# Performance work log

Measured on AMD Instinct MI355X. Metric: run time of the kernel, lower is better.

The kernel has to match this reference:

```python
import jax, jax.numpy as jnp
import numpy as np

N = 40000          # nodes
E = 400000         # edges (avg degree 10)
MUL0, MUL1 = 64, 32   # 64x0e + 32x1o
RAD, HID = 8, 64      # fc_neurons = [8, 64]
WNUM = 192            # tp.weight_numel = 64+64+32+32
NUM_NEIGHBORS = 10.0
INV3 = 1.0 / np.sqrt(3.0)   # wigner coeff for 1o x 1o -> 0e


def _lin(s, v, Ws, Wv, attr):
    """FullyConnectedTensorProduct(x, 1x0e attr) == per-irrep linear, fan-in normalized."""
    out_s = (s @ Ws) * attr * (1.0 / np.sqrt(Ws.shape[0]))
    out_v = jnp.einsum('nud,uv->nvd', v, Wv) * attr[..., None] * (1.0 / np.sqrt(Wv.shape[0]))
    return out_s, out_v


def setup_inputs() -> dict:
    key = jax.random.key(0)
    ks = jax.random.split(key, 16)
    return {
        'node_input':   jax.random.normal(ks[0], (N, MUL0 + 3 * MUL1), jnp.float32),
        'node_attr':    jnp.ones((N, 1), jnp.float32),
        'edge_attr':    jax.random.normal(ks[1], (E, 4), jnp.float32),   # 1x0e + 1x1o
        'edge_scalars': jax.random.uniform(ks[2], (E, RAD), jnp.float32),
        'W_sc_s': jax.random.normal(ks[3], (MUL0, MUL0), jnp.float32),
        'W_sc_v': jax.random.normal(ks[4], (MUL1, MUL1), jnp.float32),
        'W1_s':   jax.random.normal(ks[5], (MUL0, MUL0), jnp.float32),
        'W1_v':   jax.random.normal(ks[6], (MUL1, MUL1), jnp.float32),
        'W2_s':   jax.random.normal(ks[7], (MUL0 + MUL1, MUL0), jnp.float32),
        'W2_v':   jax.random.normal(ks[8], (MUL0 + MUL1, MUL1), jnp.float32),
        'W3':     jax.random.normal(ks[9], (MUL0 + MUL1, 1), jnp.float32),
        'fcW1':   jax.random.normal(ks[10], (RAD, HID), jnp.float32),
        'fcW2':   jax.random.normal(ks[11], (HID, WNUM), jnp.float32),
        'edge_src': jax.random.randint(ks[12], (E,), 0, N, jnp.int32),
        'edge_dst': jax.random.randint(ks[13], (E,), 0, N, jnp.int32),
    }


def reference(node_input, node_attr, edge_attr, edge_scalars,
              W_sc_s, W_sc_v, W1_s, W1_v, W2_s, W2_v, W3, fcW1, fcW2,
              edge_src, edge_dst):
    n = node_input.shape[0]
    s_in = node_input[:, :MUL0]                       # (N, 64)   0e
    v_in = node_input[:, MUL0:].reshape(n, MUL1, 3)   # (N, 32,3) 1o

    # self connection + first linear (FCTP with 1x0e attr)
    sc_s, sc_v = _lin(s_in, v_in, W_sc_s, W_sc_v, node_attr)
    f_s,  f_v  = _lin(s_in, v_in, W1_s,  W1_v,  node_attr)

    # radial MLP -> per-edge tensor-product weights (silu, fan-in normalized)
    h = jax.nn.silu(edge_scalars @ fcW1 * (1.0 / np.sqrt(RAD)))
    w = h @ fcW2 * (1.0 / np.sqrt(HID))               # (E, 192)
    wA, wB, wC, wD = w[:, :64], w[:, 64:128], w[:, 128:160], w[:, 160:192]

    # gather source node features
    xs = f_s[edge_src]                                # (E, 64)
    xv = f_v[edge_src]                                # (E, 32, 3)
    y0 = edge_attr[:, :1]                             # (E, 1)  0e
    y1 = edge_attr[:, 1:4]                            # (E, 3)  1o

    # 'uvu' tensor-product paths -> irreps_mid = 64x0e + 32x0e + 64x1o + 32x1o
    outA = wA * xs * y0                                            # 0e x 0e -> 0e
    outD = wD * jnp.einsum('eud,ed->eu', xv, y1) * INV3            # 1o x 1o -> 0e
    outB = wB[:, :, None] * xs[:, :, None] * y1[:, None, :]       # 0e x 1o -> 1o
    outC = wC[:, :, None] * xv * y0[:, :, None]                    # 1o x 0e -> 1o
    edge_feat = jnp.concatenate(
        [outA, outD, outB.reshape(-1, MUL0 * 3), outC.reshape(-1, MUL1 * 3)], axis=1)  # (E, 384)

    # scatter_add into destination nodes, normalized by sqrt(num_neighbors)
    agg = jax.ops.segment_sum(edge_feat, edge_dst, num_segments=n)
    agg = agg * (1.0 / np.sqrt(NUM_NEIGHBORS))

    ms = agg[:, :MUL0 + MUL1]                               # (N, 96)   0e
    mv = agg[:, MUL0 + MUL1:].reshape(n, MUL0 + MUL1, 3)    # (N, 96,3) 1o

    # lin2: mid -> output ; lin3: mid -> 0e (scalars only)
    c_s, c_v = _lin(ms, mv, W2_s, W2_v, node_attr)
    conv = jnp.concatenate([c_s, c_v.reshape(n, -1)], axis=1)
    sc   = jnp.concatenate([sc_s, sc_v.reshape(n, -1)], axis=1)
    angle = 0.1 * (ms @ W3) * node_attr * (1.0 / np.sqrt(MUL0 + MUL1))  # (N, 1)

    # sc.output_mask is all-ones here (every output irrep has a path)
    cos, sin = jnp.cos(angle), jnp.sin(angle)
    return cos * sc + sin * conv
```

## Files before the change

### kernel.cpp

```cpp
#include <hip/hip_runtime.h>
#include <math.h>

#define MUL0 64
#define MUL1 32
#define RADF 8
#define HIDF 64
#define WNUM 192
#define NODE_F 160
#define AGG_F  384

#define INV_SQRT64 0.125f
#define INV_SQRT32 0.17677669529663687f
#define INV_SQRT8  0.35355339059327373f
#define INV_SQRT96 0.10206207261596575f
#define INV_SQRT10 0.31622776601683794f
#define INV_SQRT3  0.5773502691896258f

typedef __attribute__((ext_vector_type(8))) short bf16x8;
typedef __attribute__((ext_vector_type(4))) float f32x4;

__device__ __forceinline__ float bf2f(unsigned short u) {
    return __uint_as_float((unsigned)u << 16);
}
__device__ __forceinline__ unsigned short f2bfu(float x) {
    unsigned ua = __float_as_uint(x);
    return (unsigned short)((ua + 0x7FFF + ((ua >> 16) & 1)) >> 16);
}
__device__ __forceinline__ unsigned bf16pack(float a, float b) {
    unsigned ua = __float_as_uint(a);
    unsigned ub = __float_as_uint(b);
    ua = (ua + 0x7FFF + ((ua >> 16) & 1)) >> 16;
    ub = (ub + 0x7FFF + ((ub >> 16) & 1)) >> 16;
    return ua | (ub << 16);
}
__device__ __forceinline__ int rdlane(int v, int i) {
    return __builtin_amdgcn_readlane(v, i);
}
__device__ __forceinline__ float rdlanef(float v, int i) {
    return __int_as_float(__builtin_amdgcn_readlane(__float_as_int(v), i));
}
__device__ __forceinline__ bf16x8 cvt8(float4 a, float4 b) {
    union { unsigned q[4]; bf16x8 v; } r;
    r.q[0] = bf16pack(a.x, a.y);
    r.q[1] = bf16pack(a.z, a.w);
    r.q[2] = bf16pack(b.x, b.y);
    r.q[3] = bf16pack(b.z, b.w);
    return r.v;
}

__global__ __launch_bounds__(256) void k_node_lin(
    const float* __restrict__ node_input,
    const float* __restrict__ node_attr,
    const float* __restrict__ W1_s,
    const float* __restrict__ W1_v,
    unsigned short* __restrict__ f, int N)
{
    __shared__ unsigned short s_w1s[8 * 64 * 8];
    __shared__ unsigned short s_w1v[4 * 32 * 8];
    int tid = threadIdx.x;

    for (int task = tid; task < 8 * 64; task += 256) {
        int col = task & 63, koct = task >> 6;
        const float* wp = W1_s + (size_t)(koct * 8) * MUL0 + col;
        unsigned pk0 = bf16pack(wp[0 * MUL0] * INV_SQRT64, wp[1 * MUL0] * INV_SQRT64);
        unsigned pk1 = bf16pack(wp[2 * MUL0] * INV_SQRT64, wp[3 * MUL0] * INV_SQRT64);
        unsigned pk2 = bf16pack(wp[4 * MUL0] * INV_SQRT64, wp[5 * MUL0] * INV_SQRT64);
        unsigned pk3 = bf16pack(wp[6 * MUL0] * INV_SQRT64, wp[7 * MUL0] * INV_SQRT64);
        *(uint4*)&s_w1s[task * 8] = make_uint4(pk0, pk1, pk2, pk3);
    }
    for (int task = tid; task < 4 * 32; task += 256) {
        int col = task & 31, koct = task >> 5;
        const float* wp = W1_v + (size_t)(koct * 8) * MUL1 + col;
        unsigned pk0 = bf16pack(wp[0 * MUL1] * INV_SQRT32, wp[1 * MUL1] * INV_SQRT32);
        unsigned pk1 = bf16pack(wp[2 * MUL1] * INV_SQRT32, wp[3 * MUL1] * INV_SQRT32);
        unsigned pk2 = bf16pack(wp[4 * MUL1] * INV_SQRT32, wp[5 * MUL1] * INV_SQRT32);
        unsigned pk3 = bf16pack(wp[6 * MUL1] * INV_SQRT32, wp[7 * MUL1] * INV_SQRT32);
        *(uint4*)&s_w1v[task * 8] = make_uint4(pk0, pk1, pk2, pk3);
    }
    __syncthreads();

    int lane = tid & 63;
    int wv = tid >> 6;
    int l15 = lane & 15, lh = lane >> 4;
    int ntiles = (N + 15) >> 4;

    for (int tile = blockIdx.x * 4 + wv; tile < ntiles; tile += gridDim.x * 4) {
        int n0 = tile << 4;
        int m = min(16, N - n0);
        int nrow = n0 + min(l15, m - 1);
        const float* inn = node_input + (size_t)nrow * NODE_F;

        float attr[4];
        #pragma unroll
        for (int r = 0; r < 4; ++r)
            attr[r] = node_attr[n0 + min(lh * 4 + r, m - 1)];

        bf16x8 inS[2];
        #pragma unroll
        for (int kk = 0; kk < 2; ++kk) {
            const float* p0 = inn + kk * 32 + lh * 8;
            inS[kk] = cvt8(*(const float4*)p0, *(const float4*)(p0 + 4));
        }
        #pragma unroll
        for (int cb = 0; cb < 4; ++cb) {
            f32x4 a = {0.f, 0.f, 0.f, 0.f};
            #pragma unroll
            for (int kk = 0; kk < 2; ++kk) {
                bf16x8 b = *(const bf16x8*)&s_w1s[(((kk * 4 + lh) * 64) + cb * 16 + l15) * 8];
                a = __builtin_amdgcn_mfma_f32_16x16x32_bf16(inS[kk], b, a, 0, 0, 0);
            }
            #pragma unroll
            for (int r = 0; r < 4; ++r) {
                int node = lh * 4 + r;
                if (node < m)
                    f[(size_t)(n0 + node) * NODE_F + cb * 16 + l15] = f2bfu(a[r] * attr[r]);
            }
        }

        #pragma unroll
        for (int d = 0; d < 3; ++d) {
            float t[8];
            #pragma unroll
            for (int j = 0; j < 8; ++j)
                t[j] = inn[64 + (lh * 8 + j) * 3 + d];
            bf16x8 inV = cvt8(make_float4(t[0], t[1], t[2], t[3]),
                              make_float4(t[4], t[5], t[6], t[7]));
            #pragma unroll
            for (int cb = 0; cb < 2; ++cb) {
                bf16x8 b = *(const bf16x8*)&s_w1v[((lh * 32) + cb * 16 + l15) * 8];
                f32x4 a = {0.f, 0.f, 0.f, 0.f};
                a = __builtin_amdgcn_mfma_f32_16x16x32_bf16(inV, b, a, 0, 0, 0);
                #pragma unroll
                for (int r = 0; r < 4; ++r) {
                    int node = lh * 4 + r;
                    if (node < m)
                        f[(size_t)(n0 + node) * NODE_F + 64 + d * 32 + cb * 16 + l15] =
                            f2bfu(a[r] * attr[r]);
                }
            }
        }
    }
}

__global__ void k_count(const int* __restrict__ edge_dst, int* deg, int E)
{
    int e = blockIdx.x * blockDim.x + threadIdx.x;
    if (e < E) atomicAdd(&deg[edge_dst[e]], 1);
}

__global__ __launch_bounds__(1024) void k_scan(const int* __restrict__ deg,
                                               int* __restrict__ off,
                                               int* __restrict__ cur, int N)
{
    __shared__ int swsum[16];
    __shared__ int swoff[16];
    __shared__ int sbase;
    __shared__ int stotal;
    int lane = threadIdx.x & 63, wid = threadIdx.x >> 6;
    if (threadIdx.x == 0) sbase = 0;
    __syncthreads();
    int ngroups = N >> 2;
    for (int base = 0; base < ngroups; base += 1024) {
        int g = base + threadIdx.x;
        int4 v = make_int4(0, 0, 0, 0);
        if (g < ngroups) v = ((const int4*)deg)[g];
        int s = v.x + v.y + v.z + v.w;
        int val = s;
        #pragma unroll
        for (int sh = 1; sh < 64; sh <<= 1) {
            int t = __shfl_up(val, sh);
            if (lane >= sh) val += t;
        }
        if (lane == 63) swsum[wid] = val;
        __syncthreads();
        if (threadIdx.x < 16) {
            int x = swsum[threadIdx.x];
            int xv = x;
            #pragma unroll
            for (int sh = 1; sh < 16; sh <<= 1) {
                int t = __shfl_up(xv, sh);
                if ((int)threadIdx.x >= sh) xv += t;
            }
            swoff[threadIdx.x] = xv - x;
            if (threadIdx.x == 15) stotal = xv;
        }
        __syncthreads();
        if (g < ngroups) {
            int b = sbase + swoff[wid] + (val - s);
            int4 o;
            o.x = b; o.y = b + v.x; o.z = o.y + v.y; o.w = o.z + v.z;
            ((int4*)off)[g] = o;
            ((int4*)cur)[g] = o;
        }
        __syncthreads();
        if (threadIdx.x == 0) sbase += stotal;
        __syncthreads();
    }
    if (threadIdx.x == 0) {
        int b = sbase;
        for (int i = (ngroups << 2); i < N; ++i) { off[i] = b; cur[i] = b; b += deg[i]; }
        off[N] = b;
    }
}

__global__ void k_scatter(const int* __restrict__ edge_dst,
                          int* cur, int* __restrict__ csr, int E)
{
    int e = blockIdx.x * blockDim.x + threadIdx.x;
    if (e < E) {
        int d = edge_dst[e];
        int pos = atomicAdd(&cur[d], 1);
        csr[pos] = e;
    }
}

#define FLUSH_AGG(node, AT)                                          \
    do {                                                             \
        float* an = agg + (size_t)(node) * AGG_F;                    \
        if (AT) {                                                    \
            atomicAdd(&an[lane], accA);                              \
            atomicAdd(&an[96  + lane], accB0);                       \
            atomicAdd(&an[192 + lane], accB1);                       \
            atomicAdd(&an[288 + lane], accB2);                       \
            if (lane < 32) {                                         \
                atomicAdd(&an[160 + u], accX0);                      \
                atomicAdd(&an[256 + u], accX1);                      \
                atomicAdd(&an[352 + u], accX2);                      \
            } else {                                                 \
                atomicAdd(&an[64 + u], accX0);                       \
            }                                                        \
        } else {                                                     \
            an[lane] = accA;                                         \
            an[96  + lane] = accB0;                                  \
            an[192 + lane] = accB1;                                  \
            an[288 + lane] = accB2;                                  \
            if (lane < 32) {                                         \
                an[160 + u] = accX0;                                 \
                an[256 + u] = accX1;                                 \
                an[352 + u] = accX2;                                 \
            } else {                                                 \
                an[64 + u] = accX0;                                  \
            }                                                        \
        }                                                            \
    } while (0)

__global__ __launch_bounds__(256, 3) void k_edge_fused(
    const unsigned short* __restrict__ f,
    const float* __restrict__ edge_scalars,
    const float* __restrict__ edge_attr,
    const float* __restrict__ fcW1,
    const float* __restrict__ fcW2,
    const int* __restrict__ edge_src,
    const int* __restrict__ edge_dst,
    const int* __restrict__ csr,
    const int* __restrict__ off,
    float* agg, int E)
{
    __shared__ unsigned short s_w2t[8 * 192 * 8];
    __shared__ unsigned short s_w[4][16 * 216];
    __shared__ float s_fcW1[512];

    int tid  = threadIdx.x;
    int lane = tid & 63;
    int wv   = tid >> 6;
    int l15  = lane & 15, lh = lane >> 4;
    int u    = lane & 31;

    for (int task = tid; task < 1536; task += 256) {
        int col = task % 192, oct = task / 192;
        const float* wp = fcW2 + (size_t)(oct * 8) * WNUM + col;
        unsigned pk0 = bf16pack(wp[0 * WNUM], wp[1 * WNUM]);
        unsigned pk1 = bf16pack(wp[2 * WNUM], wp[3 * WNUM]);
        unsigned pk2 = bf16pack(wp[4 * WNUM], wp[5 * WNUM]);
        unsigned pk3 = bf16pack(wp[6 * WNUM], wp[7 * WNUM]);
        *(uint4*)&s_w2t[oct * 1536 + col * 8] = make_uint4(pk0, pk1, pk2, pk3);
    }
    for (int i = tid; i < 512; i += 256)
        s_fcW1[i] = fcW1[i];
    __syncthreads();

    unsigned short* sw = s_w[wv];
    int nwt = (E + 15) >> 4;
    int stride4 = gridDim.x * 4;

    int wt = blockIdx.x * 4 + wv;
    if (wt >= nwt) return;

    int P = wt << 4;
    int m = min(16, E - P);
    int e0 = csr[P + min(l15, m - 1)];
    int src = edge_src[e0];
    int dst = edge_dst[e0];
    float4 ea = *(const float4*)(edge_attr + (size_t)e0 * 4);
    float4 es0, es1;
    {
        const float4* esp = (const float4*)(edge_scalars + (size_t)e0 * RADF);
        es0 = esp[0]; es1 = esp[1];
    }

    while (true) {
        int firstd = rdlane(dst, 0);
        int lastd  = rdlane(dst, m - 1);
        int off_first = off[firstd];
        int off_last  = off[lastd + 1];

        int wt_n = wt + stride4;
        bool hn = wt_n < nwt;
        int P_n = hn ? (wt_n << 4) : 0;
        int m_n = hn ? min(16, E - P_n) : 1;

        int e_n = csr[hn ? (P_n + min(l15, m_n - 1)) : 0];

        float xs[16], xv0[16], xv1[16], xv2[16];
        #pragma unroll
        for (int i = 0; i < 16; ++i) {
            int si = rdlane(src, i);
            const unsigned short* fb = f + (size_t)si * NODE_F;
            xs[i]  = bf2f(fb[lane]);
            xv0[i] = bf2f(fb[64 + u]);
            xv1[i] = bf2f(fb[96 + u]);
            xv2[i] = bf2f(fb[128 + u]);
        }

        float es[8] = {es0.x, es0.y, es0.z, es0.w, es1.x, es1.y, es1.z, es1.w};
        union { unsigned q[4]; bf16x8 v; } A0, A1;
        #pragma unroll
        for (int jp = 0; jp < 4; ++jp) {
            int k0 = lh * 8 + 2 * jp;
            float aL0 = 0.f, aL1 = 0.f, aH0 = 0.f, aH1 = 0.f;
            #pragma unroll
            for (int r = 0; r < 8; ++r) {
                float2 wl = *(const float2*)&s_fcW1[r * 64 + k0];
                float2 wh = *(const float2*)&s_fcW1[r * 64 + 32 + k0];
                aL0 = fmaf(es[r], wl.x, aL0);
                aL1 = fmaf(es[r], wl.y, aL1);
                aH0 = fmaf(es[r], wh.x, aH0);
                aH1 = fmaf(es[r], wh.y, aH1);
            }
            aL0 *= INV_SQRT8; aL1 *= INV_SQRT8; aH0 *= INV_SQRT8; aH1 *= INV_SQRT8;
            aL0 = aL0 / (1.f + __expf(-aL0));
            aL1 = aL1 / (1.f + __expf(-aL1));
            aH0 = aH0 / (1.f + __expf(-aH0));
            aH1 = aH1 / (1.f + __expf(-aH1));
            A0.q[jp] = bf16pack(aL0, aL1);
            A1.q[jp] = bf16pack(aH0, aH1);
        }

        int src_n = edge_src[e_n];
        int dst_n = edge_dst[e_n];
        float4 ea_n = *(const float4*)(edge_attr + (size_t)e_n * 4);
        float4 es0_n, es1_n;
        {
            const float4* espn = (const float4*)(edge_scalars + (size_t)e_n * RADF);
            es0_n = espn[0]; es1_n = espn[1];
        }

        #pragma unroll
        for (int cb = 0; cb < 12; ++cb) {
            bf16x8 b0 = *(const bf16x8*)&s_w2t[ lh      * 1536 + (cb * 16 + l15) * 8];
            bf16x8 b1 = *(const bf16x8*)&s_w2t[(4 + lh) * 1536 + (cb * 16 + l15) * 8];
            f32x4 acc = {0.f, 0.f, 0.f, 0.f};
            acc = __builtin_amdgcn_mfma_f32_16x16x32_bf16(A0.v, b0, acc, 0, 0, 0);
            acc = __builtin_amdgcn_mfma_f32_16x16x32_bf16(A1.v, b1, acc, 0, 0, 0);
            #pragma unroll
            for (int r = 0; r < 4; ++r)
                sw[(lh * 4 + r) * 216 + cb * 16 + l15] = f2bfu(acc[r] * INV_SQRT64);
        }

        float accA = 0.f, accB0 = 0.f, accB1 = 0.f, accB2 = 0.f;
        float accX0 = 0.f, accX1 = 0.f, accX2 = 0.f;
        int curd = rdlane(dst, 0);
        #pragma unroll
        for (int i = 0; i < 16; ++i) {
            if (i < m) {
                int di = rdlane(dst, i);
                if (di != curd) {
                    bool at = (curd == firstd) && (off_first < P);
                    FLUSH_AGG(curd, at);
                    accA = accB0 = accB1 = accB2 = 0.f;
                    accX0 = accX1 = accX2 = 0.f;
                    curd = di;
                }
                float eax = rdlanef(ea.x, i);
                float eay = rdlanef(ea.y, i);
                float eaz = rdlanef(ea.z, i);
                float eaw = rdlanef(ea.w, i);
                float W0 = bf2f(sw[i * 216 + lane]);
                float W1 = bf2f(sw[i * 216 + 64 + lane]);
                float W2 = bf2f(sw[i * 216 + 128 + lane]);
                accA = fmaf(W0 * xs[i], eax, accA);
                float bx = W1 * xs[i];
                accB0 = fmaf(bx, eay, accB0);
                accB1 = fmaf(bx, eaz, accB1);
                accB2 = fmaf(bx, eaw, accB2);
                if (lane < 32) {
                    float cc = W2 * eax;
                    accX0 = fmaf(cc, xv0[i], accX0);
                    accX1 = fmaf(cc, xv1[i], accX1);
                    accX2 = fmaf(cc, xv2[i], accX2);
                } else {
                    float dv = xv0[i] * eay + xv1[i] * eaz + xv2[i] * eaw;
                    accX0 = fmaf(W2 * INV_SQRT3, dv, accX0);
                }
            }
        }
        {
            bool at_fin = ((curd == firstd) && (off_first < P)) || (off_last > P + m);
            FLUSH_AGG(curd, at_fin);
        }

        if (!hn) break;
        wt = wt_n; P = P_n; m = m_n;
        src = src_n; dst = dst_n; ea = ea_n; es0 = es0_n; es1 = es1_n;
    }
}

__global__ __launch_bounds__(256) void k_out(
    const float* __restrict__ node_input,
    const float* __restrict__ node_attr,
    const float* __restrict__ agg,
    const float* __restrict__ W_sc_s,
    const float* __restrict__ W_sc_v,
    const float* __restrict__ W2_s,
    const float* __restrict__ W2_v,
    const float* __restrict__ W3,
    float* __restrict__ out, int N)
{
    __shared__ unsigned short s_w2s[12 * 64 * 8];
    __shared__ unsigned short s_wss[ 8 * 64 * 8];
    __shared__ unsigned short s_w2v[12 * 32 * 8];
    __shared__ unsigned short s_wsv[ 4 * 32 * 8];
    __shared__ unsigned short s_w3 [12 * 16 * 8];

    const float pre = INV_SQRT10 * INV_SQRT96;
    int tid = threadIdx.x;

    for (int task = tid; task < 12 * 64; task += 256) {
        int col = task & 63, koct = task >> 6;
        const float* wp = W2_s + (size_t)(koct * 8) * MUL0 + col;
        unsigned pk0 = bf16pack(wp[0 * MUL0] * pre, wp[1 * MUL0] * pre);
        unsigned pk1 = bf16pack(wp[2 * MUL0] * pre, wp[3 * MUL0] * pre);
        unsigned pk2 = bf16pack(wp[4 * MUL0] * pre, wp[5 * MUL0] * pre);
        unsigned pk3 = bf16pack(wp[6 * MUL0] * pre, wp[7 * MUL0] * pre);
        *(uint4*)&s_w2s[task * 8] = make_uint4(pk0, pk1, pk2, pk3);
    }
    for (int task = tid; task < 8 * 64; task += 256) {
        int col = task & 63, koct = task >> 6;
        const float* wp = W_sc_s + (size_t)(koct * 8) * MUL0 + col;
        unsigned pk0 = bf16pack(wp[0 * MUL0] * INV_SQRT64, wp[1 * MUL0] * INV_SQRT64);
        unsigned pk1 = bf16pack(wp[2 * MUL0] * INV_SQRT64, wp[3 * MUL0] * INV_SQRT64);
        unsigned pk2 = bf16pack(wp[4 * MUL0] * INV_SQRT64, wp[5 * MUL0] * INV_SQRT64);
        unsigned pk3 = bf16pack(wp[6 * MUL0] * INV_SQRT64, wp[7 * MUL0] * INV_SQRT64);
        *(uint4*)&s_wss[task * 8] = make_uint4(pk0, pk1, pk2, pk3);
    }
    for (int task = tid; task < 12 * 32; task += 256) {
        int col = task & 31, koct = task >> 5;
        const float* wp = W2_v + (size_t)(koct * 8) * MUL1 + col;
        unsigned pk0 = bf16pack(wp[0 * MUL1] * pre, wp[1 * MUL1] * pre);
        unsigned pk1 = bf16pack(wp[2 * MUL1] * pre, wp[3 * MUL1] * pre);
        unsigned pk2 = bf16pack(wp[4 * MUL1] * pre, wp[5 * MUL1] * pre);
        unsigned pk3 = bf16pack(wp[6 * MUL1] * pre, wp[7 * MUL1] * pre);
        *(uint4*)&s_w2v[task * 8] = make_uint4(pk0, pk1, pk2, pk3);
    }
    for (int task = tid; task < 4 * 32; task += 256) {
        int col = task & 31, koct = task >> 5;
        const float* wp = W_sc_v + (size_t)(koct * 8) * MUL1 + col;
        unsigned pk0 = bf16pack(wp[0 * MUL1] * INV_SQRT32, wp[1 * MUL1] * INV_SQRT32);
        unsigned pk1 = bf16pack(wp[2 * MUL1] * INV_SQRT32, wp[3 * MUL1] * INV_SQRT32);
        unsigned pk2 = bf16pack(wp[4 * MUL1] * INV_SQRT32, wp[5 * MUL1] * INV_SQRT32);
        unsigned pk3 = bf16pack(wp[6 * MUL1] * INV_SQRT32, wp[7 * MUL1] * INV_SQRT32);
        *(uint4*)&s_wsv[task * 8] = make_uint4(pk0, pk1, pk2, pk3);
    }
    for (int task = tid; task < 12 * 16; task += 256) {
        int col = task & 15, koct = task >> 4;
        const float sc3 = 0.1f * pre;
        unsigned pk0 = 0, pk1 = 0, pk2 = 0, pk3 = 0;
        if (col == 0) {
            const float* wp = W3 + koct * 8;
            pk0 = bf16pack(wp[0] * sc3, wp[1] * sc3);
            pk1 = bf16pack(wp[2] * sc3, wp[3] * sc3);
            pk2 = bf16pack(wp[4] * sc3, wp[5] * sc3);
            pk3 = bf16pack(wp[6] * sc3, wp[7] * sc3);
        }
        *(uint4*)&s_w3[task * 8] = make_uint4(pk0, pk1, pk2, pk3);
    }
    __syncthreads();

    int lane = tid & 63;
    int wv = tid >> 6;
    int l15 = lane & 15, lh = lane >> 4;
    int ntiles = (N + 15) >> 4;

    for (int tile = blockIdx.x * 4 + wv; tile < ntiles; tile += gridDim.x * 4) {
        int n0 = tile << 4;
        int m = min(16, N - n0);
        int nrow = n0 + min(l15, m - 1);
        const float* agn = agg + (size_t)nrow * AGG_F;
        const float* inn = node_input + (size_t)nrow * NODE_F;

        bf16x8 aggA[3], inS[2];
        #pragma unroll
        for (int kk = 0; kk < 3; ++kk) {
            const float* p0 = agn + kk * 32 + lh * 8;
            aggA[kk] = cvt8(*(const float4*)p0, *(const float4*)(p0 + 4));
        }
        #pragma unroll
        for (int kk = 0; kk < 2; ++kk) {
            const float* p0 = inn + kk * 32 + lh * 8;
            inS[kk] = cvt8(*(const float4*)p0, *(const float4*)(p0 + 4));
        }

        f32x4 convS[4], scS[4], angD = {0.f, 0.f, 0.f, 0.f};
        #pragma unroll
        for (int cb = 0; cb < 4; ++cb) {
            f32x4 a = {0.f, 0.f, 0.f, 0.f};
            #pragma unroll
            for (int kk = 0; kk < 3; ++kk) {
                bf16x8 b = *(const bf16x8*)&s_w2s[(((kk * 4 + lh) * 64) + cb * 16 + l15) * 8];
                a = __builtin_amdgcn_mfma_f32_16x16x32_bf16(aggA[kk], b, a, 0, 0, 0);
            }
            convS[cb] = a;
            f32x4 s = {0.f, 0.f, 0.f, 0.f};
            #pragma unroll
            for (int kk = 0; kk < 2; ++kk) {
                bf16x8 b = *(const bf16x8*)&s_wss[(((kk * 4 + lh) * 64) + cb * 16 + l15) * 8];
                s = __builtin_amdgcn_mfma_f32_16x16x32_bf16(inS[kk], b, s, 0, 0, 0);
            }
            scS[cb] = s;
        }
        #pragma unroll
        for (int kk = 0; kk < 3; ++kk) {
            bf16x8 b = *(const bf16x8*)&s_w3[(((kk * 4 + lh) * 16) + l15) * 8];
            angD = __builtin_amdgcn_mfma_f32_16x16x32_bf16(aggA[kk], b, angD, 0, 0, 0);
        }

        float attr[4], cs[4], sn[4];
        #pragma unroll
        for (int r = 0; r < 4; ++r) {
            attr[r] = node_attr[n0 + min(lh * 4 + r, m - 1)];
            float ang = __shfl(angD[r], lane & 48) * attr[r];
            cs[r] = cosf(ang);
            sn[r] = sinf(ang);
        }

        #pragma unroll
        for (int cb = 0; cb < 4; ++cb)
            #pragma unroll
            for (int r = 0; r < 4; ++r) {
                int node = lh * 4 + r;
                if (node < m)
                    out[(size_t)(n0 + node) * NODE_F + cb * 16 + l15] =
                        attr[r] * (cs[r] * scS[cb][r] + sn[r] * convS[cb][r]);
            }

        #pragma unroll
        for (int d = 0; d < 3; ++d) {
            bf16x8 aggV[3], inV;
            #pragma unroll
            for (int kk = 0; kk < 3; ++kk) {
                const float* p0 = agn + 96 + d * 96 + kk * 32 + lh * 8;
                aggV[kk] = cvt8(*(const float4*)p0, *(const float4*)(p0 + 4));
            }
            {
                float t[8];
                #pragma unroll
                for (int j = 0; j < 8; ++j)
                    t[j] = inn[64 + (lh * 8 + j) * 3 + d];
                inV = cvt8(make_float4(t[0], t[1], t[2], t[3]),
                           make_float4(t[4], t[5], t[6], t[7]));
            }
            #pragma unroll
            for (int cb = 0; cb < 2; ++cb) {
                f32x4 a = {0.f, 0.f, 0.f, 0.f};
                #pragma unroll
                for (int kk = 0; kk < 3; ++kk) {
                    bf16x8 b = *(const bf16x8*)&s_w2v[(((kk * 4 + lh) * 32) + cb * 16 + l15) * 8];
                    a = __builtin_amdgcn_mfma_f32_16x16x32_bf16(aggV[kk], b, a, 0, 0, 0);
                }
                f32x4 s = {0.f, 0.f, 0.f, 0.f};
                {
                    bf16x8 b = *(const bf16x8*)&s_wsv[((lh * 32) + cb * 16 + l15) * 8];
                    s = __builtin_amdgcn_mfma_f32_16x16x32_bf16(inV, b, s, 0, 0, 0);
                }
                #pragma unroll
                for (int r = 0; r < 4; ++r) {
                    int node = lh * 4 + r;
                    if (node < m)
                        out[(size_t)(n0 + node) * NODE_F + 64 + (cb * 16 + l15) * 3 + d] =
                            attr[r] * (cs[r] * s[r] + sn[r] * a[r]);
                }
            }
        }
    }
}

extern "C" void kernel_launch(void* const* d_in, const int* in_sizes, int n_in,
                              void* d_out, int out_size, void* d_ws, size_t ws_size,
                              hipStream_t stream)
{
    const float* node_input   = (const float*)d_in[0];
    const float* node_attr    = (const float*)d_in[1];
    const float* edge_attr    = (const float*)d_in[2];
    const float* edge_scalars = (const float*)d_in[3];
    const float* W_sc_s       = (const float*)d_in[4];
    const float* W_sc_v       = (const float*)d_in[5];
    const float* W1_s         = (const float*)d_in[6];
    const float* W1_v         = (const float*)d_in[7];
    const float* W2_s         = (const float*)d_in[8];
    const float* W2_v         = (const float*)d_in[9];
    const float* W3           = (const float*)d_in[10];
    const float* fcW1         = (const float*)d_in[11];
    const float* fcW2         = (const float*)d_in[12];
    const int*   edge_src     = (const int*)d_in[13];
    const int*   edge_dst     = (const int*)d_in[14];
    float* out = (float*)d_out;

    const int N = in_sizes[1];
    const int E = in_sizes[13];

    char* p = (char*)d_ws;
    float* agg = (float*)p;            p += (size_t)N * AGG_F * sizeof(float);
    unsigned short* fbf = (unsigned short*)p;  p += (size_t)N * NODE_F * sizeof(unsigned short);
    int*   deg = (int*)p;              p += (size_t)N * sizeof(int);
    int*   cur = (int*)p;              p += (size_t)N * sizeof(int);
    int*   csr = (int*)p;              p += (size_t)E * sizeof(int);
    int*   off = (int*)p;              p += (size_t)(N + 1) * sizeof(int);

    hipMemsetAsync(deg, 0, (size_t)N * sizeof(int), stream);
    hipMemsetAsync(agg, 0, (size_t)N * AGG_F * sizeof(float), stream);

    int eb = (E + 255) / 256;
    k_count<<<eb, 256, 0, stream>>>(edge_dst, deg, E);
    k_scan<<<1, 1024, 0, stream>>>(deg, off, cur, N);
    k_scatter<<<eb, 256, 0, stream>>>(edge_dst, cur, csr, E);

    int ntiles = (N + 15) / 16;
    int gridL = (ntiles + 3) / 4;
    k_node_lin<<<gridL, 256, 0, stream>>>(node_input, node_attr, W1_s, W1_v, fbf, N);

    int nwt = (E + 15) / 16;
    int gridF = (nwt + 3) / 4;
    if (gridF > 1536) gridF = 1536;
    k_edge_fused<<<gridF, 256, 0, stream>>>(fbf, edge_scalars, edge_attr, fcW1, fcW2,
                                            edge_src, edge_dst, csr, off, agg, E);

    int gridO = (ntiles + 3) / 4;
    if (gridO > 640) gridO = 640;
    k_out<<<gridO, 256, 0, stream>>>(node_input, node_attr, agg,
                                     W_sc_s, W_sc_v, W2_s, W2_v, W3, out, N);
}
```

Before: 239.1 us.

## Align edge work tiles to destination boundaries to drop atomics and agg memset

```diff
diff --git a/kernel.cpp b/kernel.cpp
--- a/kernel.cpp
+++ b/kernel.cpp
@@ -148,58 +148,82 @@
     if (e < E) atomicAdd(&deg[edge_dst[e]], 1);
 }
 
-__global__ __launch_bounds__(1024) void k_scan(const int* __restrict__ deg,
-                                               int* __restrict__ off,
-                                               int* __restrict__ cur, int N)
+__global__ __launch_bounds__(1024) void k_scan_a(const int* __restrict__ deg,
+                                                 int* __restrict__ off,
+                                                 int* __restrict__ bsum, int N)
 {
     __shared__ int swsum[16];
     __shared__ int swoff[16];
+    __shared__ int stot;
+    int lane = threadIdx.x & 63, wid = threadIdx.x >> 6;
+    int ng4 = (N + 3) >> 2;
+    int g = blockIdx.x * 1024 + threadIdx.x;
+    int4 v = make_int4(0, 0, 0, 0);
+    if (g < ng4) v = ((const int4*)deg)[g];
+    int s = v.x + v.y + v.z + v.w;
+    int val = s;
+    #pragma unroll
+    for (int sh = 1; sh < 64; sh <<= 1) {
+        int t = __shfl_up(val, sh);
+        if (lane >= sh) val += t;
+    }
+    if (lane == 63) swsum[wid] = val;
+    __syncthreads();
+    if (threadIdx.x < 16) {
+        int x = swsum[threadIdx.x];
+        int xv = x;
+        #pragma unroll
+        for (int sh = 1; sh < 16; sh <<= 1) {
+            int t = __shfl_up(xv, sh);
+            if ((int)threadIdx.x >= sh) xv += t;
+        }
+        swoff[threadIdx.x] = xv - x;
+        if (threadIdx.x == 15) stot = xv;
+    }
+    __syncthreads();
+    if (g < ng4) {
+        int b0 = swoff[wid] + (val - s);
+        int4 o;
+        o.x = b0; o.y = b0 + v.x; o.z = o.y + v.y; o.w = o.z + v.z;
+        ((int4*)off)[g] = o;
+    }
+    if (threadIdx.x == 0) bsum[blockIdx.x] = stot;
+}
+
+__global__ __launch_bounds__(1024) void k_scan_b(int* __restrict__ off,
+                                                 int* __restrict__ cur,
+                                                 const int* __restrict__ bsum,
+                                                 float* __restrict__ agg,
+                                                 const int* __restrict__ deg,
+                                                 int N, int nb)
+{
     __shared__ int sbase;
-    __shared__ int stotal;
-    int lane = threadIdx.x & 63, wid = threadIdx.x >> 6;
-    if (threadIdx.x == 0) sbase = 0;
+    if (threadIdx.x == 0) {
+        int s = 0;
+        for (int j = 0; j < (int)blockIdx.x; ++j) s += bsum[j];
+        sbase = s;
+    }
     __syncthreads();
-    int ngroups = N >> 2;
-    for (int base = 0; base < ngroups; base += 1024) {
-        int g = base + threadIdx.x;
-        int4 v = make_int4(0, 0, 0, 0);
-        if (g < ngroups) v = ((const int4*)deg)[g];
-        int s = v.x + v.y + v.z + v.w;
-        int val = s;
-        #pragma unroll
-        for (int sh = 1; sh < 64; sh <<= 1) {
-            int t = __shfl_up(val, sh);
-            if (lane >= sh) val += t;
-        }
-        if (lane == 63) swsum[wid] = val;
-        __syncthreads();
-        if (threadIdx.x < 16) {
-            int x = swsum[threadIdx.x];
-            int xv = x;
-            #pragma unroll
-            for (int sh = 1; sh < 16; sh <<= 1) {
-                int t = __shfl_up(xv, sh);
-                if ((int)threadIdx.x >= sh) xv += t;
-            }
-            swoff[threadIdx.x] = xv - x;
-            if (threadIdx.x == 15) stotal = xv;
-        }
-        __syncthreads();
-        if (g < ngroups) {
-            int b = sbase + swoff[wid] + (val - s);
-            int4 o;
-            o.x = b; o.y = b + v.x; o.z = o.y + v.y; o.w = o.z + v.z;
-            ((int4*)off)[g] = o;
-            ((int4*)cur)[g] = o;
-        }
-        __syncthreads();
-        if (threadIdx.x == 0) sbase += stotal;
-        __syncthreads();
-    }
-    if (threadIdx.x == 0) {
-        int b = sbase;
-        for (int i = (ngroups << 2); i < N; ++i) { off[i] = b; cur[i] = b; b += deg[i]; }
-        off[N] = b;
+    int base = sbase;
+    int ng4 = (N + 3) >> 2;
+    int g = blockIdx.x * 1024 + threadIdx.x;
+    if (g < ng4) {
+        int4 o = ((int4*)off)[g];
+        o.x += base; o.y += base; o.z += base; o.w += base;
+        ((int4*)off)[g] = o;
+        ((int4*)cur)[g] = o;
+        int4 d = ((const int4*)deg)[g];
+        int n0 = g * 4;
+        #pragma unroll
+        for (int q = 0; q < 4; ++q) {
+            int dq = (q == 0) ? d.x : (q == 1) ? d.y : (q == 2) ? d.z : d.w;
+            int nq = n0 + q;
+            if (dq == 0 && nq < N) {
+                float4* row = (float4*)(agg + (size_t)nq * AGG_F);
+                float4 z = make_float4(0.f, 0.f, 0.f, 0.f);
+                for (int j = 0; j < AGG_F / 4; ++j) row[j] = z;
+            }
+        }
     }
 }
 
@@ -214,33 +238,31 @@
     }
 }
 
-#define FLUSH_AGG(node, AT)                                          \
+__global__ void k_cut(const int* __restrict__ csr, const int* __restrict__ edge_dst,
+                      const int* __restrict__ off, int* __restrict__ cut, int E, int G)
+{
+    int t = blockIdx.x * 256 + threadIdx.x;
+    if (t > G) return;
+    int v;
+    if (t == 0) v = 0;
+    else if (t == G) v = E;
+    else v = off[edge_dst[csr[t << 4]]];
+    cut[t] = v;
+}
+
+#define STORE_AGG(node)                                              \
     do {                                                             \
         float* an = agg + (size_t)(node) * AGG_F;                    \
-        if (AT) {                                                    \
-            atomicAdd(&an[lane], accA);                              \
-            atomicAdd(&an[96  + lane], accB0);                       \
-            atomicAdd(&an[192 + lane], accB1);                       \
-            atomicAdd(&an[288 + lane], accB2);                       \
-            if (lane < 32) {                                         \
-                atomicAdd(&an[160 + u], accX0);                      \
-                atomicAdd(&an[256 + u], accX1);                      \
-                atomicAdd(&an[352 + u], accX2);                      \
-            } else {                                                 \
-                atomicAdd(&an[64 + u], accX0);                       \
-            }                                                        \
+        an[lane] = accA;                                             \
+        an[96  + lane] = accB0;                                      \
+        an[192 + lane] = accB1;                                      \
+        an[288 + lane] = accB2;                                      \
+        if (lane < 32) {                                             \
+            an[160 + u] = accX0;                                     \
+            an[256 + u] = accX1;                                     \
+            an[352 + u] = accX2;                                     \
         } else {                                                     \
-            an[lane] = accA;                                         \
-            an[96  + lane] = accB0;                                  \
-            an[192 + lane] = accB1;                                  \
-            an[288 + lane] = accB2;                                  \
-            if (lane < 32) {                                         \
-                an[160 + u] = accX0;                                 \
-                an[256 + u] = accX1;                                 \
-                an[352 + u] = accX2;                                 \
-            } else {                                                 \
-                an[64 + u] = accX0;                                  \
-            }                                                        \
+            an[64 + u] = accX0;                                      \
         }                                                            \
     } while (0)
 
@@ -253,8 +275,8 @@
     const int* __restrict__ edge_src,
     const int* __restrict__ edge_dst,
     const int* __restrict__ csr,
-    const int* __restrict__ off,
-    float* agg, int E)
+    const int* __restrict__ cut,
+    float* __restrict__ agg, int E, int G)
 {
     __shared__ unsigned short s_w2t[8 * 192 * 8];
     __shared__ unsigned short s_w[4][16 * 216];
@@ -280,138 +302,108 @@
     __syncthreads();
 
     unsigned short* sw = s_w[wv];
-    int nwt = (E + 15) >> 4;
-    int stride4 = gridDim.x * 4;
-
-    int wt = blockIdx.x * 4 + wv;
-    if (wt >= nwt) return;
-
-    int P = wt << 4;
-    int m = min(16, E - P);
-    int e0 = csr[P + min(l15, m - 1)];
-    int src = edge_src[e0];
-    int dst = edge_dst[e0];
-    float4 ea = *(const float4*)(edge_attr + (size_t)e0 * 4);
-    float4 es0, es1;
-    {
-        const float4* esp = (const float4*)(edge_scalars + (size_t)e0 * RADF);
-        es0 = esp[0]; es1 = esp[1];
-    }
-
-    while (true) {
-        int firstd = rdlane(dst, 0);
-        int lastd  = rdlane(dst, m - 1);
-        int off_first = off[firstd];
-        int off_last  = off[lastd + 1];
-
-        int wt_n = wt + stride4;
-        bool hn = wt_n < nwt;
-        int P_n = hn ? (wt_n << 4) : 0;
-        int m_n = hn ? min(16, E - P_n) : 1;
-
-        int e_n = csr[hn ? (P_n + min(l15, m_n - 1)) : 0];
-
-        float xs[16], xv0[16], xv1[16], xv2[16];
-        #pragma unroll
-        for (int i = 0; i < 16; ++i) {
-            int si = rdlane(src, i);
-            const unsigned short* fb = f + (size_t)si * NODE_F;
-            xs[i]  = bf2f(fb[lane]);
-            xv0[i] = bf2f(fb[64 + u]);
-            xv1[i] = bf2f(fb[96 + u]);
-            xv2[i] = bf2f(fb[128 + u]);
-        }
-
-        float es[8] = {es0.x, es0.y, es0.z, es0.w, es1.x, es1.y, es1.z, es1.w};
-        union { unsigned q[4]; bf16x8 v; } A0, A1;
-        #pragma unroll
-        for (int jp = 0; jp < 4; ++jp) {
-            int k0 = lh * 8 + 2 * jp;
-            float aL0 = 0.f, aL1 = 0.f, aH0 = 0.f, aH1 = 0.f;
-            #pragma unroll
-            for (int r = 0; r < 8; ++r) {
-                float2 wl = *(const float2*)&s_fcW1[r * 64 + k0];
-                float2 wh = *(const float2*)&s_fcW1[r * 64 + 32 + k0];
-                aL0 = fmaf(es[r], wl.x, aL0);
-                aL1 = fmaf(es[r], wl.y, aL1);
-                aH0 = fmaf(es[r], wh.x, aH0);
-                aH1 = fmaf(es[r], wh.y, aH1);
-            }
-            aL0 *= INV_SQRT8; aL1 *= INV_SQRT8; aH0 *= INV_SQRT8; aH1 *= INV_SQRT8;
-            aL0 = aL0 / (1.f + __expf(-aL0));
-            aL1 = aL1 / (1.f + __expf(-aL1));
-            aH0 = aH0 / (1.f + __expf(-aH0));
-            aH1 = aH1 / (1.f + __expf(-aH1));
-            A0.q[jp] = bf16pack(aL0, aL1);
-            A1.q[jp] = bf16pack(aH0, aH1);
-        }
-
-        int src_n = edge_src[e_n];
-        int dst_n = edge_dst[e_n];
-        float4 ea_n = *(const float4*)(edge_attr + (size_t)e_n * 4);
-        float4 es0_n, es1_n;
-        {
-            const float4* espn = (const float4*)(edge_scalars + (size_t)e_n * RADF);
-            es0_n = espn[0]; es1_n = espn[1];
-        }
-
-        #pragma unroll
-        for (int cb = 0; cb < 12; ++cb) {
-            bf16x8 b0 = *(const bf16x8*)&s_w2t[ lh      * 1536 + (cb * 16 + l15) * 8];
-            bf16x8 b1 = *(const bf16x8*)&s_w2t[(4 + lh) * 1536 + (cb * 16 + l15) * 8];
-            f32x4 acc = {0.f, 0.f, 0.f, 0.f};
-            acc = __builtin_amdgcn_mfma_f32_16x16x32_bf16(A0.v, b0, acc, 0, 0, 0);
-            acc = __builtin_amdgcn_mfma_f32_16x16x32_bf16(A1.v, b1, acc, 0, 0, 0);
-            #pragma unroll
-            for (int r = 0; r < 4; ++r)
-                sw[(lh * 4 + r) * 216 + cb * 16 + l15] = f2bfu(acc[r] * INV_SQRT64);
-        }
+
+    for (int wt = blockIdx.x * 4 + wv; wt < G; wt += gridDim.x * 4) {
+        int gbeg = cut[wt], gend = cut[wt + 1];
+        if (gbeg >= gend) continue;
 
         float accA = 0.f, accB0 = 0.f, accB1 = 0.f, accB2 = 0.f;
         float accX0 = 0.f, accX1 = 0.f, accX2 = 0.f;
-        int curd = rdlane(dst, 0);
-        #pragma unroll
-        for (int i = 0; i < 16; ++i) {
-            if (i < m) {
-                int di = rdlane(dst, i);
-                if (di != curd) {
-                    bool at = (curd == firstd) && (off_first < P);
-                    FLUSH_AGG(curd, at);
-                    accA = accB0 = accB1 = accB2 = 0.f;
-                    accX0 = accX1 = accX2 = 0.f;
-                    curd = di;
+        int curd = -1;
+
+        for (int p = gbeg; p < gend; p += 16) {
+            int sz = min(16, gend - p);
+
+            int e   = csr[p + min(l15, sz - 1)];
+            int src = edge_src[e];
+            int dst = edge_dst[e];
+            float4 ea = *(const float4*)(edge_attr + (size_t)e * 4);
+            const float4* esp = (const float4*)(edge_scalars + (size_t)e * RADF);
+            float4 es0 = esp[0], es1 = esp[1];
+
+            float xs[16], xv0[16], xv1[16], xv2[16];
+            #pragma unroll
+            for (int i = 0; i < 16; ++i) {
+                int si = rdlane(src, i);
+                const unsigned short* fb = f + (size_t)si * NODE_F;
+                xs[i]  = bf2f(fb[lane]);
+                xv0[i] = bf2f(fb[64 + u]);
+                xv1[i] = bf2f(fb[96 + u]);
+                xv2[i] = bf2f(fb[128 + u]);
+            }
+
+            float es[8] = {es0.x, es0.y, es0.z, es0.w, es1.x, es1.y, es1.z, es1.w};
+            union { unsigned q[4]; bf16x8 v; } A0, A1;
+            #pragma unroll
+            for (int jp = 0; jp < 4; ++jp) {
+                int k0 = lh * 8 + 2 * jp;
+                float aL0 = 0.f, aL1 = 0.f, aH0 = 0.f, aH1 = 0.f;
+                #pragma unroll
+                for (int r = 0; r < 8; ++r) {
+                    float2 wl = *(const float2*)&s_fcW1[r * 64 + k0];
+                    float2 wh = *(const float2*)&s_fcW1[r * 64 + 32 + k0];
+                    aL0 = fmaf(es[r], wl.x, aL0);
+                    aL1 = fmaf(es[r], wl.y, aL1);
+                    aH0 = fmaf(es[r], wh.x, aH0);
+                    aH1 = fmaf(es[r], wh.y, aH1);
                 }
-                float eax = rdlanef(ea.x, i);
-                float eay = rdlanef(ea.y, i);
-                float eaz = rdlanef(ea.z, i);
-                float eaw = rdlanef(ea.w, i);
-                float W0 = bf2f(sw[i * 216 + lane]);
-                float W1 = bf2f(sw[i * 216 + 64 + lane]);
-                float W2 = bf2f(sw[i * 216 + 128 + lane]);
-                accA = fmaf(W0 * xs[i], eax, accA);
-                float bx = W1 * xs[i];
-                accB0 = fmaf(bx, eay, accB0);
-                accB1 = fmaf(bx, eaz, accB1);
-                accB2 = fmaf(bx, eaw, accB2);
-                if (lane < 32) {
-                    float cc = W2 * eax;
-                    accX0 = fmaf(cc, xv0[i], accX0);
-                    accX1 = fmaf(cc, xv1[i], accX1);
-                    accX2 = fmaf(cc, xv2[i], accX2);
-                } else {
-                    float dv = xv0[i] * eay + xv1[i] * eaz + xv2[i] * eaw;
-                    accX0 = fmaf(W2 * INV_SQRT3, dv, accX0);
+                aL0 *= INV_SQRT8; aL1 *= INV_SQRT8; aH0 *= INV_SQRT8; aH1 *= INV_SQRT8;
+                aL0 = aL0 / (1.f + __expf(-aL0));
+                aL1 = aL1 / (1.f + __expf(-aL1));
+                aH0 = aH0 / (1.f + __expf(-aH0));
+                aH1 = aH1 / (1.f + __expf(-aH1));
+                A0.q[jp] = bf16pack(aL0, aL1);
+                A1.q[jp] = bf16pack(aH0, aH1);
+            }
+
+            #pragma unroll
+            for (int cb = 0; cb < 12; ++cb) {
+                bf16x8 b0 = *(const bf16x8*)&s_w2t[ lh      * 1536 + (cb * 16 + l15) * 8];
+                bf16x8 b1 = *(const bf16x8*)&s_w2t[(4 + lh) * 1536 + (cb * 16 + l15) * 8];
+                f32x4 acc = {0.f, 0.f, 0.f, 0.f};
+                acc = __builtin_amdgcn_mfma_f32_16x16x32_bf16(A0.v, b0, acc, 0, 0, 0);
+                acc = __builtin_amdgcn_mfma_f32_16x16x32_bf16(A1.v, b1, acc, 0, 0, 0);
+                #pragma unroll
+                for (int r = 0; r < 4; ++r)
+                    sw[(lh * 4 + r) * 216 + cb * 16 + l15] = f2bfu(acc[r] * INV_SQRT64);
+            }
+
+            if (curd < 0) curd = rdlane(dst, 0);
+            #pragma unroll
+            for (int i = 0; i < 16; ++i) {
+                if (i < sz) {
+                    int di = rdlane(dst, i);
+                    if (di != curd) {
+                        STORE_AGG(curd);
+                        accA = accB0 = accB1 = accB2 = 0.f;
+                        accX0 = accX1 = accX2 = 0.f;
+                        curd = di;
+                    }
+                    float eax = rdlanef(ea.x, i);
+                    float eay = rdlanef(ea.y, i);
+                    float eaz = rdlanef(ea.z, i);
+                    float eaw = rdlanef(ea.w, i);
+                    float W0 = bf2f(sw[i * 216 + lane]);
+                    float W1 = bf2f(sw[i * 216 + 64 + lane]);
+                    float W2 = bf2f(sw[i * 216 + 128 + lane]);
+                    accA = fmaf(W0 * xs[i], eax, accA);
+                    float bx = W1 * xs[i];
+                    accB0 = fmaf(bx, eay, accB0);
+                    accB1 = fmaf(bx, eaz, accB1);
+                    accB2 = fmaf(bx, eaw, accB2);
+                    if (lane < 32) {
+                        float cc = W2 * eax;
+                        accX0 = fmaf(cc, xv0[i], accX0);
+                        accX1 = fmaf(cc, xv1[i], accX1);
+                        accX2 = fmaf(cc, xv2[i], accX2);
+                    } else {
+                        float dv = xv0[i] * eay + xv1[i] * eaz + xv2[i] * eaw;
+                        accX0 = fmaf(W2 * INV_SQRT3, dv, accX0);
+                    }
                 }
             }
         }
-        {
-            bool at_fin = ((curd == firstd) && (off_first < P)) || (off_last > P + m);
-            FLUSH_AGG(curd, at_fin);
-        }
-
-        if (!hn) break;
-        wt = wt_n; P = P_n; m = m_n;
-        src = src_n; dst = dst_n; ea = ea_n; es0 = es0_n; es1 = es1_n;
+        STORE_AGG(curd);
     }
 }
 
@@ -617,32 +609,39 @@
 
     const int N = in_sizes[1];
     const int E = in_sizes[13];
+    const int Np = (N + 3) & ~3;
+    const int G = (E + 15) / 16;
 
     char* p = (char*)d_ws;
     float* agg = (float*)p;            p += (size_t)N * AGG_F * sizeof(float);
     unsigned short* fbf = (unsigned short*)p;  p += (size_t)N * NODE_F * sizeof(unsigned short);
-    int*   deg = (int*)p;              p += (size_t)N * sizeof(int);
-    int*   cur = (int*)p;              p += (size_t)N * sizeof(int);
+    int*   deg = (int*)p;              p += (size_t)Np * sizeof(int);
+    int*   cur = (int*)p;              p += (size_t)Np * sizeof(int);
+    int*   off = (int*)p;              p += (size_t)(Np + 4) * sizeof(int);
     int*   csr = (int*)p;              p += (size_t)E * sizeof(int);
-    int*   off = (int*)p;              p += (size_t)(N + 1) * sizeof(int);
-
-    hipMemsetAsync(deg, 0, (size_t)N * sizeof(int), stream);
-    hipMemsetAsync(agg, 0, (size_t)N * AGG_F * sizeof(float), stream);
+    int*   cutb = (int*)p;             p += (size_t)(G + 1) * sizeof(int);
+    int*   bsum = (int*)p;             p += 64 * sizeof(int);
+
+    hipMemsetAsync(deg, 0, (size_t)Np * sizeof(int), stream);
 
     int eb = (E + 255) / 256;
     k_count<<<eb, 256, 0, stream>>>(edge_dst, deg, E);
-    k_scan<<<1, 1024, 0, stream>>>(deg, off, cur, N);
+
+    int ng4 = (N + 3) >> 2;
+    int nb = (ng4 + 1023) / 1024;
+    k_scan_a<<<nb, 1024, 0, stream>>>(deg, off, bsum, N);
+    k_scan_b<<<nb, 1024, 0, stream>>>(off, cur, bsum, agg, deg, N, nb);
     k_scatter<<<eb, 256, 0, stream>>>(edge_dst, cur, csr, E);
+    k_cut<<<(G + 256) / 256, 256, 0, stream>>>(csr, edge_dst, off, cutb, E, G);
 
     int ntiles = (N + 15) / 16;
     int gridL = (ntiles + 3) / 4;
     k_node_lin<<<gridL, 256, 0, stream>>>(node_input, node_attr, W1_s, W1_v, fbf, N);
 
-    int nwt = (E + 15) / 16;
-    int gridF = (nwt + 3) / 4;
+    int gridF = (G + 3) / 4;
     if (gridF > 1536) gridF = 1536;
     k_edge_fused<<<gridF, 256, 0, stream>>>(fbf, edge_scalars, edge_attr, fcW1, fcW2,
-                                            edge_src, edge_dst, csr, off, agg, E);
+                                            edge_src, edge_dst, csr, cutb, agg, E, G);
 
     int gridO = (ntiles + 3) / 4;
     if (gridO > 640) gridO = 640;
```

New measurement: 251.7 us. +5.2%, slower.
